# Kernel tuning notes

Hardware: AMD Instinct MI355X
Metric: run time of the kernel (lower is better)

Reference implementation:

```python
import jax, jax.numpy as jnp
import numpy as np

N, E, C, H = 50000, 1_600_000, 128, 128
NUM_GRAPHS = 64


def setup_inputs() -> dict:
    key = jax.random.key(0)
    ks = jax.random.split(key, 9)
    x = jax.random.normal(ks[0], (N, C), dtype=jnp.float32)
    edge_index = jax.random.randint(ks[1], (2, E), 0, N, dtype=jnp.int64)
    edge_index_neg = jax.random.randint(ks[2], (2, E), 0, N, dtype=jnp.int64)
    batch = jnp.sort(jax.random.randint(ks[3], (N,), 0, NUM_GRAPHS, dtype=jnp.int64))
    W1 = jax.random.normal(ks[4], (C, H), dtype=jnp.float32) * 0.05
    b1 = jnp.zeros((H,), dtype=jnp.float32)
    W2 = jax.random.normal(ks[5], (H, H), dtype=jnp.float32) * 0.05
    b2 = jnp.zeros((H,), dtype=jnp.float32)
    We = jax.random.normal(ks[6], (2 * H, 1), dtype=jnp.float32) * 0.05
    be = jnp.zeros((1,), dtype=jnp.float32)
    return {"x": x, "edge_index": edge_index, "edge_index_neg": edge_index_neg,
            "batch": batch, "W1": W1, "b1": b1, "W2": W2, "b2": b2,
            "We": We, "be": be}


def reference(x, edge_index, edge_index_neg, batch, W1, b1, W2, b2, We, be):
    # x_enc: Linear -> ReLU -> Linear, then outer ReLU activation (eval mode, dropout=0)
    h = jax.nn.relu(jnp.dot(x, W1) + b1)          # [N, H]
    h = jax.nn.relu(jnp.dot(h, W2) + b2)          # [N, H]
    # p_e_x(cat([q, k])) == q @ We[:H] + k @ We[H:] + be  (avoids materializing cat)
    hdim = W1.shape[1]
    Wq, Wk = We[:hdim], We[hdim:]                  # [H,1] each

    def edge_score(ei):
        q = h[ei[0]]                               # [E, H] gather
        k = h[ei[1]]                               # [E, H] gather
        return jnp.dot(q, Wq) + jnp.dot(k, Wk) + be  # [E, 1]

    e_pred_pos = edge_score(edge_index)
    e_pred_neg = edge_score(edge_index_neg)
    return (e_pred_pos, e_pred_neg, edge_index_neg)
```

## Files before the change

kernel.cpp:

```cpp
#include <hip/hip_runtime.h>

#define CDIM 128
#define HDIM 128
#define LIM  40960

typedef short bf16x8 __attribute__((ext_vector_type(8)));
typedef float f32x16 __attribute__((ext_vector_type(16)));

static __device__ __forceinline__ short f2bf(float f) {
    union { float f; unsigned u; } v; v.f = f;
    unsigned r = v.u + 0x7FFFu + ((v.u >> 16) & 1u);
    return (short)(r >> 16);
}
static __device__ __forceinline__ unsigned pack2(float a, float b) {
    return (unsigned)(unsigned short)f2bf(a) | ((unsigned)(unsigned short)f2bf(b) << 16);
}

__global__ __launch_bounds__(256, 2) void node_mfma(
    const float* __restrict__ x,
    const float* __restrict__ W1, const float* __restrict__ b1,
    const float* __restrict__ W2, const float* __restrict__ b2,
    const float* __restrict__ We,
    unsigned* __restrict__ tab, int N)
{
    __shared__ __align__(16) short wfA[2][16384];
    __shared__ __align__(16) float cv[512];

    const int tid = threadIdx.x;
    const int l   = tid & 63;
    const int col = l & 31;
    const int hi  = l >> 5;
    const int node = blockIdx.x * 128 + (tid >> 6) * 32 + col;

    const int nclamp = (node < N) ? node : (N - 1);
    const float* xb = &x[(size_t)nclamp * CDIM + hi * 8];
    float4 xr[16];
#pragma unroll
    for (int ks = 0; ks < 8; ks++) {
        xr[2 * ks]     = *(const float4*)(xb + ks * 16);
        xr[2 * ks + 1] = *(const float4*)(xb + ks * 16 + 4);
    }

#pragma unroll
    for (int t = 0; t < 16; t++) {
        int tt = t * 256 + tid;
        int layer = tt >> 11;
        int rem = tt & 2047;
        int lv = rem & 63, ks = (rem >> 6) & 7, ct = rem >> 9;
        const float* Wsrc = layer ? W2 : W1;
        int k0 = ks * 16 + 8 * (lv >> 5);
        int n  = ct * 32 + (lv & 31);
        bf16x8 wv;
#pragma unroll
        for (int j = 0; j < 8; j++) wv[j] = f2bf(Wsrc[(k0 + j) * HDIM + n]);
        *(bf16x8*)&wfA[layer][rem * 8] = wv;
    }
    for (int i = tid; i < 512; i += 256)
        cv[i] = (i < 128) ? b1[i] : (i < 256) ? b2[i - 128] : We[i - 256];

    bf16x8 af[8];
#pragma unroll
    for (int ks = 0; ks < 8; ks++) {
        float4 v0 = xr[2 * ks], v1 = xr[2 * ks + 1];
        af[ks][0] = f2bf(v0.x); af[ks][1] = f2bf(v0.y);
        af[ks][2] = f2bf(v0.z); af[ks][3] = f2bf(v0.w);
        af[ks][4] = f2bf(v1.x); af[ks][5] = f2bf(v1.y);
        af[ks][6] = f2bf(v1.z); af[ks][7] = f2bf(v1.w);
    }
    __syncthreads();

    const f32x16 zz = {0.f,0.f,0.f,0.f,0.f,0.f,0.f,0.f,0.f,0.f,0.f,0.f,0.f,0.f,0.f,0.f};

    f32x16 acc[4];
#pragma unroll
    for (int ct = 0; ct < 4; ct++) acc[ct] = zz;
#pragma unroll
    for (int ks = 0; ks < 8; ks++) {
#pragma unroll
        for (int ct = 0; ct < 4; ct++) {
            bf16x8 wfrag = *(const bf16x8*)&wfA[0][((ct * 8 + ks) * 64 + l) * 8];
            acc[ct] = __builtin_amdgcn_mfma_f32_32x32x16_bf16(wfrag, af[ks], acc[ct], 0, 0, 0);
        }
    }

    unsigned P[4][4][2], Q[4][4][2];
#pragma unroll
    for (int ct = 0; ct < 4; ct++) {
#pragma unroll
        for (int g = 0; g < 4; g++) {
            float4 bv = *(const float4*)&cv[32 * ct + 8 * g + 4 * hi];
            float h0  = fmaxf(acc[ct][4 * g + 0] + bv.x, 0.f);
            float h1v = fmaxf(acc[ct][4 * g + 1] + bv.y, 0.f);
            float h2v = fmaxf(acc[ct][4 * g + 2] + bv.z, 0.f);
            float h3v = fmaxf(acc[ct][4 * g + 3] + bv.w, 0.f);
            P[ct][g][0] = pack2(h0, h1v);
            P[ct][g][1] = pack2(h2v, h3v);
        }
    }
#pragma unroll
    for (int ct = 0; ct < 4; ct++)
#pragma unroll
        for (int g = 0; g < 4; g++)
#pragma unroll
            for (int p = 0; p < 2; p++)
                Q[ct][g][p] = (unsigned)__shfl_xor((int)P[ct][g][p], 32, 64);

    f32x16 acc2[4];
#pragma unroll
    for (int ct = 0; ct < 4; ct++) acc2[ct] = zz;
#pragma unroll
    for (int ks2 = 0; ks2 < 8; ks2++) {
        const int c  = ks2 >> 1;
        const int s2 = (ks2 & 1) * 2;
        union { bf16x8 v; unsigned u[4]; } bb;
        bb.u[0] = hi ? Q[c][s2 + 1][0] : P[c][s2][0];
        bb.u[1] = hi ? Q[c][s2 + 1][1] : P[c][s2][1];
        bb.u[2] = hi ? P[c][s2 + 1][0] : Q[c][s2][0];
        bb.u[3] = hi ? P[c][s2 + 1][1] : Q[c][s2][1];
#pragma unroll
        for (int ct = 0; ct < 4; ct++) {
            bf16x8 wfrag = *(const bf16x8*)&wfA[1][((ct * 8 + ks2) * 64 + l) * 8];
            acc2[ct] = __builtin_amdgcn_mfma_f32_32x32x16_bf16(wfrag, bb.v, acc2[ct], 0, 0, 0);
        }
    }

    float pq = 0.f, pk = 0.f;
#pragma unroll
    for (int ct = 0; ct < 4; ct++) {
#pragma unroll
        for (int g = 0; g < 4; g++) {
            float4 b2v = *(const float4*)&cv[128 + 32 * ct + 8 * g + 4 * hi];
            float4 wqv = *(const float4*)&cv[256 + 32 * ct + 8 * g + 4 * hi];
            float4 wkv = *(const float4*)&cv[384 + 32 * ct + 8 * g + 4 * hi];
            const float* b2a = (const float*)&b2v;
            const float* wqa = (const float*)&wqv;
            const float* wka = (const float*)&wkv;
#pragma unroll
            for (int i = 0; i < 4; i++) {
                float hv = fmaxf(acc2[ct][4 * g + i] + b2a[i], 0.f);
                pq = fmaf(hv, wqa[i], pq);
                pk = fmaf(hv, wka[i], pk);
            }
        }
    }
    pq += __shfl_xor(pq, 32, 64);
    pk += __shfl_xor(pk, 32, 64);
    if (hi == 0 && node < N) tab[node] = pack2(pq, pk);
}

__global__ __launch_bounds__(1024) void edge_kernel(
    const int* __restrict__ eip, const int* __restrict__ ein,
    const unsigned* __restrict__ tab, const float* __restrict__ be_p,
    float* __restrict__ out, int E)
{
    __shared__ __align__(16) unsigned lt[LIM];
    const int tid = threadIdx.x;
    const int wv = tid >> 6, ln = tid & 63;

    const uint4* tg4 = (const uint4*)tab;
#pragma unroll
    for (int t = 0; t < LIM / 4 / 1024; t++) {
        int c = (t * 16 + wv) * 64;
        __builtin_amdgcn_global_load_lds(
            (const __attribute__((address_space(1))) void*)(tg4 + c + ln),
            (__attribute__((address_space(3))) void*)((char*)lt + (size_t)c * 16),
            16, 0, 0);
    }
    __builtin_amdgcn_sched_barrier(0);

    const int U = E >> 2;
    const int chunk = (U + gridDim.x - 1) / gridDim.x;
    const int ustart = blockIdx.x * chunk;
    const int uend = min(U, ustart + chunk);

    const int4* eip4 = (const int4*)eip;
    const int4* ein4 = (const int4*)ein;
    float4* out4 = (float4*)out;

    const int u0 = ustart + tid, u1 = u0 + 1024;
    const bool v0 = u0 < uend, v1 = u1 < uend;
    int4 ns0 = {0,0,0,0}, nd0 = {0,0,0,0}, ns1 = {0,0,0,0}, nd1 = {0,0,0,0};
    if (v0) {
        ns0 = ein4[u0]; nd0 = ein4[U + u0];
        out4[2 * U + u0] = make_float4((float)ns0.x, (float)ns0.y, (float)ns0.z, (float)ns0.w);
        out4[3 * U + u0] = make_float4((float)nd0.x, (float)nd0.y, (float)nd0.z, (float)nd0.w);
    }
    if (v1) {
        ns1 = ein4[u1]; nd1 = ein4[U + u1];
        out4[2 * U + u1] = make_float4((float)ns1.x, (float)ns1.y, (float)ns1.z, (float)ns1.w);
        out4[3 * U + u1] = make_float4((float)nd1.x, (float)nd1.y, (float)nd1.z, (float)nd1.w);
    }
    __syncthreads();

    const float be = be_p[0];
#define GATHER(i) ((i) < LIM ? lt[i] : tab[i])
#define SCORE(us, ud) (__uint_as_float((us) << 16) + __uint_as_float((ud) & 0xFFFF0000u) + be)

    if (v0) {
        int4 ps = eip4[u0], pd = eip4[U + u0];
        unsigned a0 = GATHER(ps.x), a1 = GATHER(ps.y), a2 = GATHER(ps.z), a3 = GATHER(ps.w);
        unsigned b0 = GATHER(pd.x), b1 = GATHER(pd.y), b2 = GATHER(pd.z), b3 = GATHER(pd.w);
        unsigned c0 = GATHER(ns0.x), c1 = GATHER(ns0.y), c2 = GATHER(ns0.z), c3 = GATHER(ns0.w);
        unsigned d0 = GATHER(nd0.x), d1 = GATHER(nd0.y), d2 = GATHER(nd0.z), d3 = GATHER(nd0.w);
        out4[u0]     = make_float4(SCORE(a0,b0), SCORE(a1,b1), SCORE(a2,b2), SCORE(a3,b3));
        out4[U + u0] = make_float4(SCORE(c0,d0), SCORE(c1,d1), SCORE(c2,d2), SCORE(c3,d3));
    }
    if (v1) {
        int4 ps = eip4[u1], pd = eip4[U + u1];
        unsigned a0 = GATHER(ps.x), a1 = GATHER(ps.y), a2 = GATHER(ps.z), a3 = GATHER(ps.w);
        unsigned b0 = GATHER(pd.x), b1 = GATHER(pd.y), b2 = GATHER(pd.z), b3 = GATHER(pd.w);
        unsigned c0 = GATHER(ns1.x), c1 = GATHER(ns1.y), c2 = GATHER(ns1.z), c3 = GATHER(ns1.w);
        unsigned d0 = GATHER(nd1.x), d1 = GATHER(nd1.y), d2 = GATHER(nd1.z), d3 = GATHER(nd1.w);
        out4[u1]     = make_float4(SCORE(a0,b0), SCORE(a1,b1), SCORE(a2,b2), SCORE(a3,b3));
        out4[U + u1] = make_float4(SCORE(c0,d0), SCORE(c1,d1), SCORE(c2,d2), SCORE(c3,d3));
    }
#undef GATHER
#undef SCORE
}

extern "C" void kernel_launch(void* const* d_in, const int* in_sizes, int n_in,
                              void* d_out, int out_size, void* d_ws, size_t ws_size,
                              hipStream_t stream) {
    const float* x   = (const float*)d_in[0];
    const int*   eip = (const int*)d_in[1];
    const int*   ein = (const int*)d_in[2];
    const float* W1  = (const float*)d_in[4];
    const float* b1  = (const float*)d_in[5];
    const float* W2  = (const float*)d_in[6];
    const float* b2  = (const float*)d_in[7];
    const float* We  = (const float*)d_in[8];
    const float* be  = (const float*)d_in[9];

    const int N = in_sizes[0] / CDIM;
    const int E = in_sizes[1] / 2;

    unsigned* tab = (unsigned*)d_ws;

    node_mfma<<<(N + 127) / 128, 256, 0, stream>>>(x, W1, b1, W2, b2, We, tab, N);
    edge_kernel<<<256, 1024, 0, stream>>>(eip, ein, tab, be, (float*)d_out, E);
}
```

Measured before the change: 29.70 us.

## Move negative-edge index cast into node kernel tail via atomic work queue

The int-to-float copy of edge_index_neg into the output moves out of the edge kernel and into the tail of the node MLP kernel. Blocks there claim 2048-vector chunks through a global atomic counter, so the copy overlaps the compute-bound node phase. The edge kernel shrinks to 512 threads per block and walks its range in a loop that prefetches the next iteration's indices. The counter is reset by the edge kernel for the next call, which relies on stream ordering and adds atomic and barrier overhead to every node block.

```diff
diff --git a/kernel.cpp b/kernel.cpp
--- a/kernel.cpp
+++ b/kernel.cpp
@@ -6,6 +6,8 @@
 
 typedef short bf16x8 __attribute__((ext_vector_type(8)));
 typedef float f32x16 __attribute__((ext_vector_type(16)));
+
+__device__ int g_cast_counter = 0;
 
 static __device__ __forceinline__ short f2bf(float f) {
     union { float f; unsigned u; } v; v.f = f;
@@ -21,10 +23,12 @@
     const float* __restrict__ W1, const float* __restrict__ b1,
     const float* __restrict__ W2, const float* __restrict__ b2,
     const float* __restrict__ We,
-    unsigned* __restrict__ tab, int N)
+    const int* __restrict__ ein,
+    unsigned* __restrict__ tab, float* __restrict__ out, int N, int E)
 {
     __shared__ __align__(16) short wfA[2][16384];
     __shared__ __align__(16) float cv[512];
+    __shared__ int s_chunk;
 
     const int tid = threadIdx.x;
     const int l   = tid & 63;
@@ -146,9 +150,32 @@
     pq += __shfl_xor(pq, 32, 64);
     pk += __shfl_xor(pk, 32, 64);
     if (hi == 0 && node < N) tab[node] = pack2(pq, pk);
-}
-
-__global__ __launch_bounds__(1024) void edge_kernel(
+
+    {
+        const int C4  = (E * 2) >> 2;
+        const int NCH = (C4 + 2047) >> 11;
+        const int4* ein4 = (const int4*)ein;
+        float4* o4 = (float4*)out + (E >> 1);
+        for (;;) {
+            __syncthreads();
+            if (tid == 0) s_chunk = atomicAdd(&g_cast_counter, 1);
+            __syncthreads();
+            int c = s_chunk;
+            if (c >= NCH) break;
+            int base = c << 11;
+#pragma unroll
+            for (int i = 0; i < 8; i++) {
+                int idx = base + i * 256 + tid;
+                if (idx < C4) {
+                    int4 v = ein4[idx];
+                    o4[idx] = make_float4((float)v.x, (float)v.y, (float)v.z, (float)v.w);
+                }
+            }
+        }
+    }
+}
+
+__global__ __launch_bounds__(512) void edge_kernel(
     const int* __restrict__ eip, const int* __restrict__ ein,
     const unsigned* __restrict__ tab, const float* __restrict__ be_p,
     float* __restrict__ out, int E)
@@ -157,10 +184,12 @@
     const int tid = threadIdx.x;
     const int wv = tid >> 6, ln = tid & 63;
 
+    if (blockIdx.x == 0 && tid == 0) atomicExch(&g_cast_counter, 0);
+
     const uint4* tg4 = (const uint4*)tab;
 #pragma unroll
-    for (int t = 0; t < LIM / 4 / 1024; t++) {
-        int c = (t * 16 + wv) * 64;
+    for (int t = 0; t < LIM / 4 / 512; t++) {
+        int c = (t * 8 + wv) * 64;
         __builtin_amdgcn_global_load_lds(
             (const __attribute__((address_space(1))) void*)(tg4 + c + ln),
             (__attribute__((address_space(3))) void*)((char*)lt + (size_t)c * 16),
@@ -177,42 +206,30 @@
     const int4* ein4 = (const int4*)ein;
     float4* out4 = (float4*)out;
 
-    const int u0 = ustart + tid, u1 = u0 + 1024;
-    const bool v0 = u0 < uend, v1 = u1 < uend;
-    int4 ns0 = {0,0,0,0}, nd0 = {0,0,0,0}, ns1 = {0,0,0,0}, nd1 = {0,0,0,0};
-    if (v0) {
-        ns0 = ein4[u0]; nd0 = ein4[U + u0];
-        out4[2 * U + u0] = make_float4((float)ns0.x, (float)ns0.y, (float)ns0.z, (float)ns0.w);
-        out4[3 * U + u0] = make_float4((float)nd0.x, (float)nd0.y, (float)nd0.z, (float)nd0.w);
-    }
-    if (v1) {
-        ns1 = ein4[u1]; nd1 = ein4[U + u1];
-        out4[2 * U + u1] = make_float4((float)ns1.x, (float)ns1.y, (float)ns1.z, (float)ns1.w);
-        out4[3 * U + u1] = make_float4((float)nd1.x, (float)nd1.y, (float)nd1.z, (float)nd1.w);
-    }
+    int u = ustart + tid;
+    bool v = u < uend;
+    int4 ps = {0,0,0,0}, pd = {0,0,0,0}, ns = {0,0,0,0}, nd = {0,0,0,0};
+    if (v) { ps = eip4[u]; pd = eip4[U + u]; ns = ein4[u]; nd = ein4[U + u]; }
+
     __syncthreads();
 
     const float be = be_p[0];
 #define GATHER(i) ((i) < LIM ? lt[i] : tab[i])
 #define SCORE(us, ud) (__uint_as_float((us) << 16) + __uint_as_float((ud) & 0xFFFF0000u) + be)
-
-    if (v0) {
-        int4 ps = eip4[u0], pd = eip4[U + u0];
+    while (v) {
+        int un = u + 512;
+        bool vn = un < uend;
+        int4 ps2 = {0,0,0,0}, pd2 = {0,0,0,0}, ns2 = {0,0,0,0}, nd2 = {0,0,0,0};
+        if (vn) { ps2 = eip4[un]; pd2 = eip4[U + un]; ns2 = ein4[un]; nd2 = ein4[U + un]; }
+
         unsigned a0 = GATHER(ps.x), a1 = GATHER(ps.y), a2 = GATHER(ps.z), a3 = GATHER(ps.w);
         unsigned b0 = GATHER(pd.x), b1 = GATHER(pd.y), b2 = GATHER(pd.z), b3 = GATHER(pd.w);
-        unsigned c0 = GATHER(ns0.x), c1 = GATHER(ns0.y), c2 = GATHER(ns0.z), c3 = GATHER(ns0.w);
-        unsigned d0 = GATHER(nd0.x), d1 = GATHER(nd0.y), d2 = GATHER(nd0.z), d3 = GATHER(nd0.w);
-        out4[u0]     = make_float4(SCORE(a0,b0), SCORE(a1,b1), SCORE(a2,b2), SCORE(a3,b3));
-        out4[U + u0] = make_float4(SCORE(c0,d0), SCORE(c1,d1), SCORE(c2,d2), SCORE(c3,d3));
-    }
-    if (v1) {
-        int4 ps = eip4[u1], pd = eip4[U + u1];
-        unsigned a0 = GATHER(ps.x), a1 = GATHER(ps.y), a2 = GATHER(ps.z), a3 = GATHER(ps.w);
-        unsigned b0 = GATHER(pd.x), b1 = GATHER(pd.y), b2 = GATHER(pd.z), b3 = GATHER(pd.w);
-        unsigned c0 = GATHER(ns1.x), c1 = GATHER(ns1.y), c2 = GATHER(ns1.z), c3 = GATHER(ns1.w);
-        unsigned d0 = GATHER(nd1.x), d1 = GATHER(nd1.y), d2 = GATHER(nd1.z), d3 = GATHER(nd1.w);
-        out4[u1]     = make_float4(SCORE(a0,b0), SCORE(a1,b1), SCORE(a2,b2), SCORE(a3,b3));
-        out4[U + u1] = make_float4(SCORE(c0,d0), SCORE(c1,d1), SCORE(c2,d2), SCORE(c3,d3));
+        unsigned c0 = GATHER(ns.x), c1 = GATHER(ns.y), c2 = GATHER(ns.z), c3 = GATHER(ns.w);
+        unsigned d0 = GATHER(nd.x), d1 = GATHER(nd.y), d2 = GATHER(nd.z), d3 = GATHER(nd.w);
+        out4[u]     = make_float4(SCORE(a0,b0), SCORE(a1,b1), SCORE(a2,b2), SCORE(a3,b3));
+        out4[U + u] = make_float4(SCORE(c0,d0), SCORE(c1,d1), SCORE(c2,d2), SCORE(c3,d3));
+
+        u = un; v = vn; ps = ps2; pd = pd2; ns = ns2; nd = nd2;
     }
 #undef GATHER
 #undef SCORE
@@ -236,6 +253,7 @@
 
     unsigned* tab = (unsigned*)d_ws;
 
-    node_mfma<<<(N + 127) / 128, 256, 0, stream>>>(x, W1, b1, W2, b2, We, tab, N);
-    edge_kernel<<<256, 1024, 0, stream>>>(eip, ein, tab, be, (float*)d_out, E);
-}
+    node_mfma<<<(N + 127) / 128, 256, 0, stream>>>(x, W1, b1, W2, b2, We, ein,
+                                                   tab, (float*)d_out, N, E);
+    edge_kernel<<<256, 512, 0, stream>>>(eip, ein, tab, be, (float*)d_out, E);
+}
```

Result: slower. 35.42 us (+19.3%).

## Quantize per-node edge projections to int8 so the whole table fits in LDS

Applied to the files above, without the earlier changes.

The node kernel now computes the global max magnitude of the q and k projections, using a wave reduction plus atomicMax into a zeroed scales buffer. The edge kernel quantizes the bf16 table into a packed int8 pair per node held entirely in shared memory. This removes the global-memory fallback gathers for node indices beyond the old LDS capacity and halves the table footprint. In exchange it adds a memset launch, a per-block conversion pass, and int8 quantization error on the edge scores, which may exceed output tolerance.

```diff
diff --git a/kernel.cpp b/kernel.cpp
--- a/kernel.cpp
+++ b/kernel.cpp
@@ -2,7 +2,7 @@
 
 #define CDIM 128
 #define HDIM 128
-#define LIM  40960
+#define LIM8 51200
 
 typedef short bf16x8 __attribute__((ext_vector_type(8)));
 typedef float f32x16 __attribute__((ext_vector_type(16)));
@@ -21,7 +21,7 @@
     const float* __restrict__ W1, const float* __restrict__ b1,
     const float* __restrict__ W2, const float* __restrict__ b2,
     const float* __restrict__ We,
-    unsigned* __restrict__ tab, int N)
+    unsigned* __restrict__ tab, unsigned* __restrict__ scales, int N)
 {
     __shared__ __align__(16) short wfA[2][16384];
     __shared__ __align__(16) float cv[512];
@@ -146,27 +146,49 @@
     pq += __shfl_xor(pq, 32, 64);
     pk += __shfl_xor(pk, 32, 64);
     if (hi == 0 && node < N) tab[node] = pack2(pq, pk);
+
+    float aq = fabsf(pq), ak = fabsf(pk);
+#pragma unroll
+    for (int s = 1; s < 64; s <<= 1) {
+        aq = fmaxf(aq, __shfl_xor(aq, s, 64));
+        ak = fmaxf(ak, __shfl_xor(ak, s, 64));
+    }
+    if (l == 0) {
+        atomicMax(&scales[0], __float_as_uint(aq));
+        atomicMax(&scales[1], __float_as_uint(ak));
+    }
 }
 
 __global__ __launch_bounds__(1024) void edge_kernel(
     const int* __restrict__ eip, const int* __restrict__ ein,
-    const unsigned* __restrict__ tab, const float* __restrict__ be_p,
-    float* __restrict__ out, int E)
+    const unsigned* __restrict__ tab, const unsigned* __restrict__ scales,
+    const float* __restrict__ be_p, float* __restrict__ out, int N, int E)
 {
-    __shared__ __align__(16) unsigned lt[LIM];
+    __shared__ __align__(16) unsigned short lt8[LIM8];
     const int tid = threadIdx.x;
-    const int wv = tid >> 6, ln = tid & 63;
+
+    const float scq = fmaxf(__uint_as_float(scales[0]), 1e-20f);
+    const float sck = fmaxf(__uint_as_float(scales[1]), 1e-20f);
+    const float invq = 127.0f / scq, invk = 127.0f / sck;
+    const float dq = scq / 127.0f,  dk = sck / 127.0f;
 
     const uint4* tg4 = (const uint4*)tab;
-#pragma unroll
-    for (int t = 0; t < LIM / 4 / 1024; t++) {
-        int c = (t * 16 + wv) * 64;
-        __builtin_amdgcn_global_load_lds(
-            (const __attribute__((address_space(1))) void*)(tg4 + c + ln),
-            (__attribute__((address_space(3))) void*)((char*)lt + (size_t)c * 16),
-            16, 0, 0);
-    }
-    __builtin_amdgcn_sched_barrier(0);
+    const int NP4 = (N + 3) >> 2;
+    for (int i = tid; i < NP4; i += 1024) {
+        uint4 u = tg4[i];
+        unsigned long long o = 0;
+#pragma unroll
+        for (int jj = 0; jj < 4; jj++) {
+            unsigned w = (jj == 0) ? u.x : (jj == 1) ? u.y : (jj == 2) ? u.z : u.w;
+            float sq = __uint_as_float(w << 16);
+            float sk = __uint_as_float(w & 0xFFFF0000u);
+            int qi = (int)rintf(sq * invq);
+            int ki = (int)rintf(sk * invk);
+            unsigned short pp = (unsigned short)((qi & 0xFF) | ((ki & 0xFF) << 8));
+            o |= (unsigned long long)pp << (16 * jj);
+        }
+        *(unsigned long long*)&lt8[i * 4] = o;
+    }
 
     const int U = E >> 2;
     const int chunk = (U + gridDim.x - 1) / gridDim.x;
@@ -193,28 +215,23 @@
     __syncthreads();
 
     const float be = be_p[0];
-#define GATHER(i) ((i) < LIM ? lt[i] : tab[i])
-#define SCORE(us, ud) (__uint_as_float((us) << 16) + __uint_as_float((ud) & 0xFFFF0000u) + be)
+#define SCORE(si, di) (fmaf((float)(int)(signed char)(lt8[si] & 0xFF), dq, \
+                       fmaf((float)(int)(signed char)(lt8[di] >> 8), dk, be)))
 
     if (v0) {
         int4 ps = eip4[u0], pd = eip4[U + u0];
-        unsigned a0 = GATHER(ps.x), a1 = GATHER(ps.y), a2 = GATHER(ps.z), a3 = GATHER(ps.w);
-        unsigned b0 = GATHER(pd.x), b1 = GATHER(pd.y), b2 = GATHER(pd.z), b3 = GATHER(pd.w);
-        unsigned c0 = GATHER(ns0.x), c1 = GATHER(ns0.y), c2 = GATHER(ns0.z), c3 = GATHER(ns0.w);
-        unsigned d0 = GATHER(nd0.x), d1 = GATHER(nd0.y), d2 = GATHER(nd0.z), d3 = GATHER(nd0.w);
-        out4[u0]     = make_float4(SCORE(a0,b0), SCORE(a1,b1), SCORE(a2,b2), SCORE(a3,b3));
-        out4[U + u0] = make_float4(SCORE(c0,d0), SCORE(c1,d1), SCORE(c2,d2), SCORE(c3,d3));
+        out4[u0]     = make_float4(SCORE(ps.x, pd.x), SCORE(ps.y, pd.y),
+                                   SCORE(ps.z, pd.z), SCORE(ps.w, pd.w));
+        out4[U + u0] = make_float4(SCORE(ns0.x, nd0.x), SCORE(ns0.y, nd0.y),
+                                   SCORE(ns0.z, nd0.z), SCORE(ns0.w, nd0.w));
     }
     if (v1) {
         int4 ps = eip4[u1], pd = eip4[U + u1];
-        unsigned a0 = GATHER(ps.x), a1 = GATHER(ps.y), a2 = GATHER(ps.z), a3 = GATHER(ps.w);
-        unsigned b0 = GATHER(pd.x), b1 = GATHER(pd.y), b2 = GATHER(pd.z), b3 = GATHER(pd.w);
-        unsigned c0 = GATHER(ns1.x), c1 = GATHER(ns1.y), c2 = GATHER(ns1.z), c3 = GATHER(ns1.w);
-        unsigned d0 = GATHER(nd1.x), d1 = GATHER(nd1.y), d2 = GATHER(nd1.z), d3 = GATHER(nd1.w);
-        out4[u1]     = make_float4(SCORE(a0,b0), SCORE(a1,b1), SCORE(a2,b2), SCORE(a3,b3));
-        out4[U + u1] = make_float4(SCORE(c0,d0), SCORE(c1,d1), SCORE(c2,d2), SCORE(c3,d3));
-    }
-#undef GATHER
+        out4[u1]     = make_float4(SCORE(ps.x, pd.x), SCORE(ps.y, pd.y),
+                                   SCORE(ps.z, pd.z), SCORE(ps.w, pd.w));
+        out4[U + u1] = make_float4(SCORE(ns1.x, nd1.x), SCORE(ns1.y, nd1.y),
+                                   SCORE(ns1.z, nd1.z), SCORE(ns1.w, nd1.w));
+    }
 #undef SCORE
 }
 
@@ -234,8 +251,13 @@
     const int N = in_sizes[0] / CDIM;
     const int E = in_sizes[1] / 2;
 
-    unsigned* tab = (unsigned*)d_ws;
-
-    node_mfma<<<(N + 127) / 128, 256, 0, stream>>>(x, W1, b1, W2, b2, We, tab, N);
-    edge_kernel<<<256, 1024, 0, stream>>>(eip, ein, tab, be, (float*)d_out, E);
-}
+    char* ws = (char*)d_ws;
+    unsigned* tab    = (unsigned*)ws;
+    unsigned* scales = (unsigned*)(ws + 200704);
+
+    hipMemsetAsync(scales, 0, 8, stream);
+    node_mfma<<<(N + 127) / 128, 256, 0, stream>>>(x, W1, b1, W2, b2, We,
+                                                   tab, scales, N);
+    edge_kernel<<<256, 1024, 0, stream>>>(eip, ein, tab, scales, be,
+                                          (float*)d_out, N, E);
+}
```

After: 68.45 us. 2.31x slower.
